# Performance work log

Hardware: AMD Instinct MI355X
Metric: run time of the kernel (lower is better)

The kernel has to match this reference:

```python
import jax, jax.numpy as jnp
import numpy as np


def setup_inputs() -> dict:
    key = jax.random.key(0)
    ks = jax.random.split(key, 5)
    B, L, C = 32, 64, 128      # batch, set_size, input_channels
    D, O = 512, 256            # mlp hidden dim, output_channels
    L2 = L * L                 # 4096 = set_size**2 (FSPool set size)
    x = jax.random.normal(ks[0], (B, L, C), dtype=jnp.float32)
    # Linear weights stored as [in, out]; kaiming-ish scaling
    w1 = jax.random.normal(ks[1], (2 * C, D), dtype=jnp.float32) / np.sqrt(2 * C)
    b1 = jnp.zeros((D,), dtype=jnp.float32)
    w2 = jax.random.normal(ks[2], (D, O), dtype=jnp.float32) / np.sqrt(D)
    b2 = jnp.zeros((O,), dtype=jnp.float32)
    # FSPool weight [set_size**2, out_channels], kaiming_normal fan_out linear
    pool_w = jax.random.normal(ks[3], (L2, O), dtype=jnp.float32) / np.sqrt(O)
    return {"x": x, "w1": w1, "b1": b1, "w2": w2, "b2": b2, "pool_w": pool_w}


def reference(x, w1, b1, w2, b2, pool_w):
    B, L, C = x.shape
    # create_pairs + concat: [B, L, L, 2C] -> flatten to [B, L*L, 2C]
    a = jnp.broadcast_to(x[:, :, None, :], (B, L, L, C))
    b = jnp.broadcast_to(x[:, None, :, :], (B, L, L, C))
    pairs = jnp.concatenate([a, b], axis=-1).reshape(B, L * L, 2 * C)
    # 2-layer MLP
    h = jax.nn.relu(pairs @ w1 + b1)            # [B, L^2, D]
    y = h @ w2 + b2                             # [B, L^2, O]
    # FSPool: featurewise sort over set dim, then weighted sum
    y = jnp.sort(y, axis=1)                     # [B, L^2, O]
    return jnp.einsum('nlc,lc->nc', y, pool_w)  # [B, O]
```

## Files before the change

kernel.cpp:

```cpp
#include <hip/hip_runtime.h>
#include <hip/hip_bf16.h>
#include <hip/hip_fp16.h>

typedef __attribute__((ext_vector_type(4))) float f32x4;
typedef _Float16 h8 __attribute__((ext_vector_type(8)));
typedef int i32x4 __attribute__((ext_vector_type(4)));
typedef _Float16 h2 __attribute__((ext_vector_type(2)));

static __device__ __forceinline__ h2 ih2(int x) { return __builtin_bit_cast(h2, x); }
static __device__ __forceinline__ unsigned pkrtz(float lo, float hi) {
  return __builtin_bit_cast(unsigned, __builtin_amdgcn_cvt_pkrtz(lo, hi));
}
static __device__ __forceinline__ int pkmin(int x, int y) {
  int d; asm("v_pk_min_f16 %0, %1, %2" : "=v"(d) : "v"(x), "v"(y)); return d;
}
static __device__ __forceinline__ int pkmax(int x, int y) {
  int d; asm("v_pk_max_f16 %0, %1, %2" : "=v"(d) : "v"(x), "v"(y)); return d;
}
static __device__ __forceinline__ int pkadd(int x, int y) {
  int d; asm("v_pk_add_f16 %0, %1, %2" : "=v"(d) : "v"(x), "v"(y)); return d;
}


__global__ __launch_bounds__(256) void k_uv(const float* __restrict__ x,
                                            const float* __restrict__ w1,
                                            const float* __restrict__ b1,
                                            _Float16* __restrict__ u,
                                            _Float16* __restrict__ v) {
  __shared__ float xs[8 * 128];
  int t = threadIdx.x;
  int r0 = blockIdx.x * 8;
  ((float4*)xs)[t] = ((const float4*)(x + (size_t)r0 * 128))[t];
  __syncthreads();
  int d1 = t, d2 = t + 256;
  float au0[8], au1[8], av0[8], av1[8];
  float bb1 = b1[d1], bb2 = b1[d2];
#pragma unroll
  for (int r = 0; r < 8; ++r) { au0[r] = bb1; au1[r] = bb2; av0[r] = 0.f; av1[r] = 0.f; }
#pragma unroll 4
  for (int c = 0; c < 128; ++c) {
    float wu1 = w1[c * 512 + d1];
    float wu2 = w1[c * 512 + d2];
    float wv1 = w1[(c + 128) * 512 + d1];
    float wv2 = w1[(c + 128) * 512 + d2];
#pragma unroll
    for (int r = 0; r < 8; ++r) {
      float xv = xs[r * 128 + c];
      au0[r] = fmaf(xv, wu1, au0[r]);
      au1[r] = fmaf(xv, wu2, au1[r]);
      av0[r] = fmaf(xv, wv1, av0[r]);
      av1[r] = fmaf(xv, wv2, av1[r]);
    }
  }
#pragma unroll
  for (int r = 0; r < 8; ++r) {
    u[(size_t)(r0 + r) * 512 + d1] = (_Float16)au0[r];
    u[(size_t)(r0 + r) * 512 + d2] = (_Float16)au1[r];
    v[(size_t)(r0 + r) * 512 + d1] = (_Float16)av0[r];
    v[(size_t)(r0 + r) * 512 + d2] = (_Float16)av1[r];
  }
}

__global__ __launch_bounds__(256) void k_w2t(const float* __restrict__ w2,
                                             _Float16* __restrict__ w2t) {
  int n = blockIdx.x;
  int t = threadIdx.x;
  w2t[(size_t)n * 512 + t]       = (_Float16)w2[(size_t)t * 256 + n];
  w2t[(size_t)n * 512 + t + 256] = (_Float16)w2[(size_t)(t + 256) * 256 + n];
}

__global__ __launch_bounds__(256) void k_pwt(const float* __restrict__ pw,
                                             float* __restrict__ pwt) {
  int o = blockIdx.x;
  int t = threadIdx.x;
#pragma unroll
  for (int it = 0; it < 16; ++it) {
    int l = it * 256 + t;
    pwt[(size_t)o * 4096 + l] = pw[(size_t)l * 256 + o];
  }
}

__global__ __launch_bounds__(256, 2) void k_gemm(const _Float16* __restrict__ u,
                                                 const _Float16* __restrict__ v,
                                                 const _Float16* __restrict__ w2t,
                                                 const float* __restrict__ b2,
                                                 unsigned short* __restrict__ yt) {
  __shared__ char vl[64 * 1024];
  __shared__ char ulm[4 * 1024];
  int t = threadIdx.x;
  int n0 = blockIdx.x;
  int bid = (n0 & 7) * 64 + (n0 >> 3);
  int b = bid >> 4, ig = bid & 15;
  {
    const char* vsrc = (const char*)(v + (size_t)b * 64 * 512);
#pragma unroll
    for (int it = 0; it < 16; ++it) {
      int f = it * 4096 + t * 16;
      uint4 d = *(const uint4*)(vsrc + f);
      int row = f >> 10;
      *(uint4*)(vl + (f ^ ((row & 7) << 4))) = d;
    }
    const char* usrc = (const char*)(u + (size_t)(b * 64 + ig * 4) * 512);
    int f = t * 16;
    *(uint4*)(ulm + f) = *(const uint4*)(usrc + f);
  }
  __syncthreads();
  int w = t >> 6, l = t & 63, lr = l & 15, lg = l >> 4;
  const _Float16* bptr[4];
  float bias[4];
#pragma unroll
  for (int ni = 0; ni < 4; ++ni) {
    int col = w * 64 + ni * 16 + lr;
    bptr[ni] = w2t + (size_t)col * 512 + lg * 8;
    bias[ni] = b2[col];
  }
#pragma unroll 1
  for (int ih = 0; ih < 2; ++ih) {
    f32x4 acc[2][4][4];
#pragma unroll
    for (int ip = 0; ip < 2; ++ip)
#pragma unroll
      for (int mi = 0; mi < 4; ++mi)
#pragma unroll
        for (int ni = 0; ni < 4; ++ni) {
          float bv = bias[ni];
          f32x4 ci = {bv, bv, bv, bv};
          acc[ip][mi][ni] = ci;
        }
#pragma unroll 2
    for (int kk = 0; kk < 16; ++kk) {
      h8 bfv[4];
#pragma unroll
      for (int ni = 0; ni < 4; ++ni) bfv[ni] = *(const h8*)(bptr[ni] + kk * 32);
      i32x4 vf[4];
#pragma unroll
      for (int mi = 0; mi < 4; ++mi) {
        int row = mi * 16 + lr;
        int fb = row * 1024 + kk * 64 + lg * 16;
        vf[mi] = *(const i32x4*)(vl + (fb ^ ((row & 7) << 4)));
      }
#pragma unroll
      for (int ip = 0; ip < 2; ++ip) {
        i32x4 uf = *(const i32x4*)(ulm + (ih * 2 + ip) * 1024 + kk * 64 + lg * 16);
#pragma unroll
        for (int mi = 0; mi < 4; ++mi) {
          i32x4 aw;
#pragma unroll
          for (int q = 0; q < 4; ++q) aw[q] = pkmax(pkadd(uf[q], vf[mi][q]), 0);
          h8 af = __builtin_bit_cast(h8, aw);
#pragma unroll
          for (int ni = 0; ni < 4; ++ni)
            acc[ip][mi][ni] =
                __builtin_amdgcn_mfma_f32_16x16x32_f16(af, bfv[ni], acc[ip][mi][ni], 0, 0, 0);
        }
      }
    }
#pragma unroll
    for (int ip = 0; ip < 2; ++ip) {
      int i = ig * 4 + ih * 2 + ip;
#pragma unroll
      for (int ni = 0; ni < 4; ++ni) {
        int col = w * 64 + ni * 16 + lr;
        unsigned short* colbase = yt + (size_t)(b * 256 + col) * 4096 + (size_t)i * 64;
#pragma unroll
        for (int mi = 0; mi < 4; ++mi) {
          f32x4 vv = acc[ip][mi][ni];
          uint2 st;
          st.x = pkrtz(vv[0], vv[1]);
          st.y = pkrtz(vv[2], vv[3]);
          *(uint2*)(colbase + mi * 16 + lg * 4) = st;
        }
      }
    }
  }
}

#define DPP_X1 0xB1
#define DPP_X2 0x4E
#define DPP_X3 0x1B
#define DPP_X7 0x141
#define DPP_X8 0x128
#define DPP_XF 0x140

template <int M, int HB>
static __device__ __forceinline__ void intra(int* a) {
#pragma unroll
  for (int e = 0; e < 64; ++e)
    if ((e & HB) == 0) {
      int f = e ^ M;
      int lo = pkmin(a[e], a[f]);
      int hi = pkmax(a[e], a[f]);
      a[e] = lo;
      a[f] = hi;
    }
}

template <int CTRL>
static __device__ __forceinline__ void cdpp(int* a, bool km) {
#pragma unroll
  for (int e = 0; e < 64; ++e) {
    int r = __builtin_amdgcn_mov_dpp(a[e], CTRL, 0xf, 0xf, true);
    int mn = pkmin(a[e], r), mx = pkmax(a[e], r);
    a[e] = km ? mn : mx;
  }
}

template <int CTRL>
static __device__ __forceinline__ void fdpp(int* a, bool km) {
#pragma unroll
  for (int e = 0; e < 32; ++e) {
    int f = e ^ 63;
    int r0 = __builtin_amdgcn_mov_dpp(a[f], CTRL, 0xf, 0xf, true);
    int r1 = __builtin_amdgcn_mov_dpp(a[e], CTRL, 0xf, 0xf, true);
    int mn0 = pkmin(a[e], r0), mx0 = pkmax(a[e], r0);
    int mn1 = pkmin(a[f], r1), mx1 = pkmax(a[f], r1);
    a[e] = km ? mn0 : mx0;
    a[f] = km ? mn1 : mx1;
  }
}

static __device__ __forceinline__ void cbp(int* a, int tm, bool km, int l) {
  int paddr = ((l ^ tm) & 63) << 2;
#pragma unroll
  for (int e = 0; e < 64; ++e) {
    int r = __builtin_amdgcn_ds_bpermute(paddr, a[e]);
    int mn = pkmin(a[e], r), mx = pkmax(a[e], r);
    a[e] = km ? mn : mx;
  }
}

static __device__ __forceinline__ void fbp(int* a, int tm, bool km, int l) {
  int paddr = ((l ^ tm) & 63) << 2;
#pragma unroll
  for (int e = 0; e < 32; ++e) {
    int f = e ^ 63;
    int r0 = __builtin_amdgcn_ds_bpermute(paddr, a[f]);
    int r1 = __builtin_amdgcn_ds_bpermute(paddr, a[e]);
    int mn0 = pkmin(a[e], r0), mx0 = pkmax(a[e], r0);
    int mn1 = pkmin(a[f], r1), mx1 = pkmax(a[f], r1);
    a[e] = km ? mn0 : mx0;
    a[f] = km ? mn1 : mx1;
  }
}

__global__ __launch_bounds__(256, 3) void k_sortpool(const unsigned short* __restrict__ yt,
                                                     const float* __restrict__ pwt,
                                                     float* __restrict__ out) {
  int t = threadIdx.x;
  int l = t & 63;
  int g = blockIdx.x * 4 + (t >> 6);
  int b = g >> 7, p = g & 127;
  int o0 = p * 2, o1 = o0 + 1;
  const uint4* c0 = (const uint4*)(yt + (size_t)(b * 256 + o0) * 4096 + l * 64);
  const uint4* c1 = (const uint4*)(yt + (size_t)(b * 256 + o1) * 4096 + l * 64);
  int a[64];
#pragma unroll
  for (int q = 0; q < 8; ++q) {
    uint4 x0 = c0[q], x1 = c1[q];
    unsigned w0[4] = {x0.x, x0.y, x0.z, x0.w};
    unsigned w1[4] = {x1.x, x1.y, x1.z, x1.w};
#pragma unroll
    for (int r = 0; r < 4; ++r) {
      a[q * 8 + 2 * r]     = (int)((w0[r] & 0xffffu) | (w1[r] << 16));
      a[q * 8 + 2 * r + 1] = (int)((w0[r] >> 16) | (w1[r] & 0xffff0000u));
    }
  }
  intra<1, 1>(a);
  intra<3, 2>(a); intra<1, 1>(a);
  intra<7, 4>(a); intra<2, 2>(a); intra<1, 1>(a);
  intra<15, 8>(a); intra<4, 4>(a); intra<2, 2>(a); intra<1, 1>(a);
  intra<31, 16>(a); intra<8, 8>(a); intra<4, 4>(a); intra<2, 2>(a); intra<1, 1>(a);
  intra<63, 32>(a); intra<16, 16>(a); intra<8, 8>(a); intra<4, 4>(a);
  intra<2, 2>(a); intra<1, 1>(a);
#define CLEAN6 intra<32, 32>(a); intra<16, 16>(a); intra<8, 8>(a); \
               intra<4, 4>(a); intra<2, 2>(a); intra<1, 1>(a)
  fdpp<DPP_X1>(a, !(l & 1)); CLEAN6;
  fdpp<DPP_X3>(a, !(l & 2)); cdpp<DPP_X1>(a, !(l & 1)); CLEAN6;
  fdpp<DPP_X7>(a, !(l & 4)); cdpp<DPP_X2>(a, !(l & 2)); cdpp<DPP_X1>(a, !(l & 1)); CLEAN6;
  fdpp<DPP_XF>(a, !(l & 8)); cbp(a, 4, !(l & 4), l);
  cdpp<DPP_X2>(a, !(l & 2)); cdpp<DPP_X1>(a, !(l & 1)); CLEAN6;
  fbp(a, 31, !(l & 16), l); cdpp<DPP_X8>(a, !(l & 8)); cbp(a, 4, !(l & 4), l);
  cdpp<DPP_X2>(a, !(l & 2)); cdpp<DPP_X1>(a, !(l & 1)); CLEAN6;
  fbp(a, 63, !(l & 32), l); cbp(a, 16, !(l & 16), l); cdpp<DPP_X8>(a, !(l & 8));
  cbp(a, 4, !(l & 4), l); cdpp<DPP_X2>(a, !(l & 2)); cdpp<DPP_X1>(a, !(l & 1)); CLEAN6;
#undef CLEAN6
  const float4* pw0 = (const float4*)(pwt + (size_t)o0 * 4096 + l * 64);
  const float4* pw1 = (const float4*)(pwt + (size_t)o1 * 4096 + l * 64);
  float s0 = 0.f, s1 = 0.f;
#pragma unroll
  for (int q = 0; q < 16; ++q) {
    float4 w0 = pw0[q], w1 = pw1[q];
    float k0[4] = {w0.x, w0.y, w0.z, w0.w};
    float k1[4] = {w1.x, w1.y, w1.z, w1.w};
#pragma unroll
    for (int r = 0; r < 4; ++r) {
      h2 v2 = ih2(a[q * 4 + r]);
      s0 = fmaf((float)v2[0], k0[r], s0);
      s1 = fmaf((float)v2[1], k1[r], s1);
    }
  }
#pragma unroll
  for (int off = 32; off > 0; off >>= 1) {
    s0 += __shfl_xor(s0, off);
    s1 += __shfl_xor(s1, off);
  }
  if (l == 0) {
    out[b * 256 + o0] = s0;
    out[b * 256 + o1] = s1;
  }
}

extern "C" void kernel_launch(void* const* d_in, const int* in_sizes, int n_in,
                              void* d_out, int out_size, void* d_ws, size_t ws_size,
                              hipStream_t stream) {
  const float* x  = (const float*)d_in[0];
  const float* w1 = (const float*)d_in[1];
  const float* b1 = (const float*)d_in[2];
  const float* w2 = (const float*)d_in[3];
  const float* b2 = (const float*)d_in[4];
  const float* pw = (const float*)d_in[5];
  char* ws = (char*)d_ws;
  _Float16* u   = (_Float16*)ws;
  _Float16* v   = (_Float16*)(ws + (2u << 20));
  _Float16* w2t = (_Float16*)(ws + (4u << 20));
  float*    pwt = (float*)(ws + (5u << 20));
  unsigned short* yt = (unsigned short*)(ws + (9u << 20));
  float* out = (float*)d_out;

  k_uv<<<dim3(256), dim3(256), 0, stream>>>(x, w1, b1, u, v);
  k_w2t<<<dim3(256), dim3(256), 0, stream>>>(w2, w2t);
  k_pwt<<<dim3(256), dim3(256), 0, stream>>>(pw, pwt);
  k_gemm<<<dim3(512), dim3(256), 0, stream>>>(u, v, w2t, b2, yt);
  k_sortpool<<<dim3(1024), dim3(256), 0, stream>>>(yt, pwt, out);
}
```

Measured before the change: 155.0 us.

## Split each sort across two wavefronts with LDS exchange to cut register pressure

The bitonic sort of 4096 packed fp16 pairs now uses 128 threads holding 32 elements each, where it previously used one 64-lane wavefront holding 64 elements per lane. The cross-wavefront merge stage goes through shared memory with a swizzled layout and a barrier, and the final pooled sums are combined across the two waves in LDS. The aim is to halve the per-thread register array so more waves fit per CU and latency is better hidden. The cost is extra LDS traffic, two block barriers and a larger grid of smaller blocks.

```diff
diff --git a/kernel.cpp b/kernel.cpp
--- a/kernel.cpp
+++ b/kernel.cpp
@@ -185,7 +185,7 @@
 template <int M, int HB>
 static __device__ __forceinline__ void intra(int* a) {
 #pragma unroll
-  for (int e = 0; e < 64; ++e)
+  for (int e = 0; e < 32; ++e)
     if ((e & HB) == 0) {
       int f = e ^ M;
       int lo = pkmin(a[e], a[f]);
@@ -198,7 +198,7 @@
 template <int CTRL>
 static __device__ __forceinline__ void cdpp(int* a, bool km) {
 #pragma unroll
-  for (int e = 0; e < 64; ++e) {
+  for (int e = 0; e < 32; ++e) {
     int r = __builtin_amdgcn_mov_dpp(a[e], CTRL, 0xf, 0xf, true);
     int mn = pkmin(a[e], r), mx = pkmax(a[e], r);
     a[e] = km ? mn : mx;
@@ -208,8 +208,8 @@
 template <int CTRL>
 static __device__ __forceinline__ void fdpp(int* a, bool km) {
 #pragma unroll
-  for (int e = 0; e < 32; ++e) {
-    int f = e ^ 63;
+  for (int e = 0; e < 16; ++e) {
+    int f = e ^ 31;
     int r0 = __builtin_amdgcn_mov_dpp(a[f], CTRL, 0xf, 0xf, true);
     int r1 = __builtin_amdgcn_mov_dpp(a[e], CTRL, 0xf, 0xf, true);
     int mn0 = pkmin(a[e], r0), mx0 = pkmax(a[e], r0);
@@ -222,7 +222,7 @@
 static __device__ __forceinline__ void cbp(int* a, int tm, bool km, int l) {
   int paddr = ((l ^ tm) & 63) << 2;
 #pragma unroll
-  for (int e = 0; e < 64; ++e) {
+  for (int e = 0; e < 32; ++e) {
     int r = __builtin_amdgcn_ds_bpermute(paddr, a[e]);
     int mn = pkmin(a[e], r), mx = pkmax(a[e], r);
     a[e] = km ? mn : mx;
@@ -232,8 +232,8 @@
 static __device__ __forceinline__ void fbp(int* a, int tm, bool km, int l) {
   int paddr = ((l ^ tm) & 63) << 2;
 #pragma unroll
-  for (int e = 0; e < 32; ++e) {
-    int f = e ^ 63;
+  for (int e = 0; e < 16; ++e) {
+    int f = e ^ 31;
     int r0 = __builtin_amdgcn_ds_bpermute(paddr, a[f]);
     int r1 = __builtin_amdgcn_ds_bpermute(paddr, a[e]);
     int mn0 = pkmin(a[e], r0), mx0 = pkmax(a[e], r0);
@@ -243,19 +243,21 @@
   }
 }
 
-__global__ __launch_bounds__(256, 3) void k_sortpool(const unsigned short* __restrict__ yt,
-                                                     const float* __restrict__ pwt,
-                                                     float* __restrict__ out) {
+__global__ __launch_bounds__(128) void k_sortpool(const unsigned short* __restrict__ yt,
+                                                  const float* __restrict__ pwt,
+                                                  float* __restrict__ out) {
+  __shared__ int sx[128 * 32];
+  __shared__ float red[4];
   int t = threadIdx.x;
   int l = t & 63;
-  int g = blockIdx.x * 4 + (t >> 6);
+  int g = blockIdx.x;
   int b = g >> 7, p = g & 127;
   int o0 = p * 2, o1 = o0 + 1;
-  const uint4* c0 = (const uint4*)(yt + (size_t)(b * 256 + o0) * 4096 + l * 64);
-  const uint4* c1 = (const uint4*)(yt + (size_t)(b * 256 + o1) * 4096 + l * 64);
-  int a[64];
-#pragma unroll
-  for (int q = 0; q < 8; ++q) {
+  const uint4* c0 = (const uint4*)(yt + (size_t)(b * 256 + o0) * 4096 + t * 32);
+  const uint4* c1 = (const uint4*)(yt + (size_t)(b * 256 + o1) * 4096 + t * 32);
+  int a[32];
+#pragma unroll
+  for (int q = 0; q < 4; ++q) {
     uint4 x0 = c0[q], x1 = c1[q];
     unsigned w0[4] = {x0.x, x0.y, x0.z, x0.w};
     unsigned w1[4] = {x1.x, x1.y, x1.z, x1.w};
@@ -270,25 +272,38 @@
   intra<7, 4>(a); intra<2, 2>(a); intra<1, 1>(a);
   intra<15, 8>(a); intra<4, 4>(a); intra<2, 2>(a); intra<1, 1>(a);
   intra<31, 16>(a); intra<8, 8>(a); intra<4, 4>(a); intra<2, 2>(a); intra<1, 1>(a);
-  intra<63, 32>(a); intra<16, 16>(a); intra<8, 8>(a); intra<4, 4>(a);
-  intra<2, 2>(a); intra<1, 1>(a);
-#define CLEAN6 intra<32, 32>(a); intra<16, 16>(a); intra<8, 8>(a); \
-               intra<4, 4>(a); intra<2, 2>(a); intra<1, 1>(a)
-  fdpp<DPP_X1>(a, !(l & 1)); CLEAN6;
-  fdpp<DPP_X3>(a, !(l & 2)); cdpp<DPP_X1>(a, !(l & 1)); CLEAN6;
-  fdpp<DPP_X7>(a, !(l & 4)); cdpp<DPP_X2>(a, !(l & 2)); cdpp<DPP_X1>(a, !(l & 1)); CLEAN6;
-  fdpp<DPP_XF>(a, !(l & 8)); cbp(a, 4, !(l & 4), l);
-  cdpp<DPP_X2>(a, !(l & 2)); cdpp<DPP_X1>(a, !(l & 1)); CLEAN6;
-  fbp(a, 31, !(l & 16), l); cdpp<DPP_X8>(a, !(l & 8)); cbp(a, 4, !(l & 4), l);
-  cdpp<DPP_X2>(a, !(l & 2)); cdpp<DPP_X1>(a, !(l & 1)); CLEAN6;
-  fbp(a, 63, !(l & 32), l); cbp(a, 16, !(l & 16), l); cdpp<DPP_X8>(a, !(l & 8));
-  cbp(a, 4, !(l & 4), l); cdpp<DPP_X2>(a, !(l & 2)); cdpp<DPP_X1>(a, !(l & 1)); CLEAN6;
-#undef CLEAN6
-  const float4* pw0 = (const float4*)(pwt + (size_t)o0 * 4096 + l * 64);
-  const float4* pw1 = (const float4*)(pwt + (size_t)o1 * 4096 + l * 64);
+#define CLEAN5 intra<16, 16>(a); intra<8, 8>(a); intra<4, 4>(a); \
+               intra<2, 2>(a); intra<1, 1>(a)
+  fdpp<DPP_X1>(a, !(t & 1)); CLEAN5;
+  fdpp<DPP_X3>(a, !(t & 2)); cdpp<DPP_X1>(a, !(t & 1)); CLEAN5;
+  fdpp<DPP_X7>(a, !(t & 4)); cdpp<DPP_X2>(a, !(t & 2)); cdpp<DPP_X1>(a, !(t & 1)); CLEAN5;
+  fdpp<DPP_XF>(a, !(t & 8)); cbp(a, 4, !(t & 4), l);
+  cdpp<DPP_X2>(a, !(t & 2)); cdpp<DPP_X1>(a, !(t & 1)); CLEAN5;
+  fbp(a, 31, !(t & 16), l); cdpp<DPP_X8>(a, !(t & 8)); cbp(a, 4, !(t & 4), l);
+  cdpp<DPP_X2>(a, !(t & 2)); cdpp<DPP_X1>(a, !(t & 1)); CLEAN5;
+  fbp(a, 63, !(t & 32), l); cbp(a, 16, !(t & 16), l); cdpp<DPP_X8>(a, !(t & 8));
+  cbp(a, 4, !(t & 4), l); cdpp<DPP_X2>(a, !(t & 2)); cdpp<DPP_X1>(a, !(t & 1)); CLEAN5;
+  {
+#pragma unroll
+    for (int e = 0; e < 32; ++e) sx[t * 32 + (e ^ (t & 31))] = a[e];
+    __syncthreads();
+    int pt = t ^ 127;
+    bool km = !(t & 64);
+#pragma unroll
+    for (int e = 0; e < 32; ++e) {
+      int r = sx[pt * 32 + ((e ^ 31) ^ (pt & 31))];
+      int mn = pkmin(a[e], r), mx = pkmax(a[e], r);
+      a[e] = km ? mn : mx;
+    }
+  }
+  cbp(a, 32, !(t & 32), l); cbp(a, 16, !(t & 16), l); cdpp<DPP_X8>(a, !(t & 8));
+  cbp(a, 4, !(t & 4), l); cdpp<DPP_X2>(a, !(t & 2)); cdpp<DPP_X1>(a, !(t & 1)); CLEAN5;
+#undef CLEAN5
+  const float4* pw0 = (const float4*)(pwt + (size_t)o0 * 4096 + t * 32);
+  const float4* pw1 = (const float4*)(pwt + (size_t)o1 * 4096 + t * 32);
   float s0 = 0.f, s1 = 0.f;
 #pragma unroll
-  for (int q = 0; q < 16; ++q) {
+  for (int q = 0; q < 8; ++q) {
     float4 w0 = pw0[q], w1 = pw1[q];
     float k0[4] = {w0.x, w0.y, w0.z, w0.w};
     float k1[4] = {w1.x, w1.y, w1.z, w1.w};
@@ -304,9 +319,12 @@
     s0 += __shfl_xor(s0, off);
     s1 += __shfl_xor(s1, off);
   }
-  if (l == 0) {
-    out[b * 256 + o0] = s0;
-    out[b * 256 + o1] = s1;
+  int wv = t >> 6;
+  if (l == 0) { red[wv * 2] = s0; red[wv * 2 + 1] = s1; }
+  __syncthreads();
+  if (t == 0) {
+    out[b * 256 + o0] = red[0] + red[2];
+    out[b * 256 + o1] = red[1] + red[3];
   }
 }
 
@@ -331,5 +349,5 @@
   k_w2t<<<dim3(256), dim3(256), 0, stream>>>(w2, w2t);
   k_pwt<<<dim3(256), dim3(256), 0, stream>>>(pw, pwt);
   k_gemm<<<dim3(512), dim3(256), 0, stream>>>(u, v, w2t, b2, yt);
-  k_sortpool<<<dim3(1024), dim3(256), 0, stream>>>(yt, pwt, out);
-}
+  k_sortpool<<<dim3(4096), dim3(128), 0, stream>>>(yt, pwt, out);
+}
```

Result: slower. 168.6 us (+8.8%).
